# Kernel tuning notes

Hardware: AMD Instinct MI355X
Metric: run time of the kernel (lower is better)

The kernel has to match this reference:

```python
import jax, jax.numpy as jnp
import numpy as np

CAT = 19          # category_num + 1 (last slot is the catch-all cluster)
ATT_SCALE = float(np.sqrt(200.0))


def _layernorm(x, scale, bias, eps=1e-5):
    mu = jnp.mean(x, axis=-1, keepdims=True)
    var = jnp.mean((x - mu) ** 2, axis=-1, keepdims=True)
    return (x - mu) * jax.lax.rsqrt(var + eps) * scale + bias


def setup_inputs() -> dict:
    key = jax.random.key(0)
    ks = jax.random.split(key, 16)
    B, N, H, D, A, L = 64, 16, 100, 400, 200, 2
    nodes = H + (CAT - 1)  # 118
    s = 1.0 / np.sqrt(D)
    return {
        "history_embedding": jax.random.normal(ks[0], (B, H, D), jnp.float32),
        "candidate_news_representation": jax.random.normal(ks[1], (B, N, D), jnp.float32),
        "user_history_graph": jax.random.uniform(ks[2], (B, nodes, nodes), jnp.float32) / nodes,
        "user_history_category_mask": jax.random.randint(ks[3], (B, CAT), 0, 2, jnp.int32),
        "user_history_category_indices": jax.random.randint(ks[4], (B, H), 0, CAT, jnp.int32),
        "proxy_node_embedding": jax.random.normal(ks[5], (CAT - 1, D), jnp.float32) * 0.02,
        "gcn_W": jax.random.normal(ks[6], (L, D, D), jnp.float32) * s,
        "gcn_b": jnp.zeros((L, D), jnp.float32),
        "ln_scale": jnp.ones((L, D), jnp.float32),
        "ln_bias": jnp.zeros((L, D), jnp.float32),
        "Kw": jax.random.normal(ks[7], (D, A), jnp.float32) * s,
        "Qw": jax.random.normal(ks[8], (D, A), jnp.float32) * s,
        "Qb": jnp.zeros((A,), jnp.float32),
        "affine_W": jax.random.normal(ks[9], (D, D), jnp.float32) * s,
        "affine_b": jnp.zeros((D,), jnp.float32),
        "icKw": jax.random.normal(ks[10], (D, A), jnp.float32) * s,
        "icQw": jax.random.normal(ks[11], (D, A), jnp.float32) * s,
        "icQb": jnp.zeros((A,), jnp.float32),
    }


def _forward(history_embedding, candidate_news_representation, user_history_graph,
             proxy_node_embedding, gcn_W, gcn_b, ln_scale, ln_bias,
             Kw, Qw, Qb, affine_W, affine_b, icKw, icQw, icQb,
             user_history_category_mask, user_history_category_indices):
    B, H, D = history_embedding.shape
    N = candidate_news_representation.shape[1]
    L = gcn_W.shape[0]

    # append proxy cluster nodes to the history graph nodes (dropout = identity at eval)
    he = jnp.concatenate(
        [history_embedding, jnp.broadcast_to(proxy_node_embedding[None], (B, CAT - 1, D))],
        axis=1)  # [B, 118, D]

    # GCN with residual + layernorm per layer, then global residual
    h = he
    for l in range(L):
        z = jnp.einsum('bij,bjd->bid', user_history_graph, h) @ gcn_W[l] + gcn_b[l]
        z = jax.nn.relu(z) + h
        h = _layernorm(z, ln_scale[l], ln_bias[l])
    gcn_feat = (h + he)[:, :H]  # [B, H, D]

    # intra-cluster scatter softmax over history items grouped by category
    K = gcn_feat @ Kw                                     # [B, H, A]
    Q = candidate_news_representation @ Qw + Qb           # [B, N, A]
    a = jnp.einsum('bha,bna->bnh', K, Q) / ATT_SCALE      # [B, N, H]

    onehot = jax.nn.one_hot(user_history_category_indices, CAT, dtype=a.dtype)  # [B, H, C]
    seg = onehot.astype(bool)
    neg = jnp.finfo(a.dtype).min
    # segment-max for stable softmax: [B, N, H, C] -> max over H
    seg_max = jnp.where(seg[:, None], a[..., None], neg).max(axis=2)            # [B, N, C]
    a_shift = a - jnp.einsum('bhc,bnc->bnh', onehot, seg_max)
    e = jnp.exp(a_shift)
    denom = jnp.einsum('bhc,bnc->bnh', onehot, jnp.einsum('bnh,bhc->bnc', e, onehot))
    alpha = e / denom                                                           # [B, N, H]

    # scatter-sum of attention-weighted gcn features into category clusters
    weighted = alpha[..., None] * gcn_feat[:, None]                             # [B, N, H, D]
    intra = jnp.einsum('bnhd,bhc->bncd', weighted, onehot)                      # [B, N, C, D]
    intra = jax.nn.relu(intra @ affine_W + affine_b) + intra

    # inter-cluster scaled-dot-product candidate attention (last cluster always valid)
    mask = user_history_category_mask.at[:, -1].set(1).astype(bool)[:, None, :]  # [B, 1, C]
    Kf = intra @ icKw                                                           # [B, N, C, A]
    q = candidate_news_representation @ icQw + icQb                             # [B, N, A]
    s = jnp.einsum('bnca,bna->bnc', Kf, q) / ATT_SCALE
    w = jax.nn.softmax(jnp.where(mask, s, neg), axis=-1)
    return jnp.einsum('bnc,bncd->bnd', w, intra)                                # [B, N, D]


def reference(history_embedding, candidate_news_representation, user_history_graph,
              user_history_category_mask, user_history_category_indices,
              proxy_node_embedding, gcn_W, gcn_b, ln_scale, ln_bias,
              Kw, Qw, Qb, affine_W, affine_b, icKw, icQw, icQb):
    return _forward(history_embedding, candidate_news_representation, user_history_graph,
                    proxy_node_embedding, gcn_W, gcn_b, ln_scale, ln_bias,
                    Kw, Qw, Qb, affine_W, affine_b, icKw, icQw, icQb,
                    user_history_category_mask, user_history_category_indices)
```

## Files before the change

### kernel.cpp

```cpp
#include <hip/hip_runtime.h>
#include <hip/hip_bf16.h>
#include <math.h>

#define BB 64
#define NN 16
#define HH 100
#define DD 400
#define AA 200
#define CATN 19
#define NODES 118
#define BN (BB*NODES)
#define BH (BB*HH)
#define ATT_INV 0.07071067811865475f

typedef __attribute__((ext_vector_type(4))) float f32x4;
typedef __attribute__((ext_vector_type(8))) short s16x8;

__device__ __forceinline__ unsigned short f2bf(float f) {
  union { float f; unsigned int u; } v; v.f = f;
  unsigned int r = v.u + 0x7FFFu + ((v.u >> 16) & 1u);
  return (unsigned short)(r >> 16);
}
__device__ __forceinline__ float bf2f(unsigned short u) {
  union { unsigned int i; float f; } v; v.i = ((unsigned int)u) << 16; return v.f;
}

__global__ __launch_bounds__(256) void k_toT_he(const float* __restrict__ hist,
    const float* __restrict__ proxy, float* __restrict__ he,
    unsigned short* __restrict__ T) {
  __shared__ float t_sh[64][129];
  const int b = blockIdx.x / 7, dt = blockIdx.x % 7;
  const int d0 = dt * 64;
  const int tid = threadIdx.x;
  const int dc = tid & 63, jr = tid >> 6;
  for (int j0 = 0; j0 < 128; j0 += 4) {
    int j = j0 + jr, d = d0 + dc;
    float v = 0.f;
    if (j < NODES && d < DD) {
      v = (j < HH) ? hist[((size_t)b * HH + j) * DD + d]
                   : proxy[(size_t)(j - HH) * DD + d];
      he[((size_t)b * NODES + j) * DD + d] = v;
    }
    t_sh[dc][j] = v;
  }
  __syncthreads();
  const int jc = tid & 127, dr2 = tid >> 7;
  for (int di = 0; di < 64; di += 2) {
    int dr = di + dr2;
    int d = d0 + dr;
    if (d < 416) T[((size_t)b * 416 + d) * 128 + jc] = f2bf(t_sh[dr][jc]);
  }
}

template<int RPB>
__global__ __launch_bounds__(256) void k_toT(const float* __restrict__ h,
    unsigned short* __restrict__ T) {
  __shared__ float t_sh[64][129];
  const int b = blockIdx.x / 7, dt = blockIdx.x % 7;
  const int d0 = dt * 64;
  const int tid = threadIdx.x;
  const int dc = tid & 63, jr = tid >> 6;
  for (int j0 = 0; j0 < 128; j0 += 4) {
    int j = j0 + jr, d = d0 + dc;
    float v = (j < RPB && d < DD) ? h[((size_t)b * RPB + j) * DD + d] : 0.f;
    t_sh[dc][j] = v;
  }
  __syncthreads();
  const int jc = tid & 127, dr2 = tid >> 7;
  for (int di = 0; di < 64; di += 2) {
    int dr = di + dr2;
    int d = d0 + dr;
    if (d < 416) T[((size_t)b * 416 + d) * 128 + jc] = f2bf(t_sh[dr][jc]);
  }
}

__global__ __launch_bounds__(256) void k_toT_gf(const float* __restrict__ h2,
    const float* __restrict__ he, float* __restrict__ gf,
    unsigned short* __restrict__ T) {
  __shared__ float t_sh[64][129];
  const int b = blockIdx.x / 7, dt = blockIdx.x % 7;
  const int d0 = dt * 64;
  const int tid = threadIdx.x;
  const int dc = tid & 63, jr = tid >> 6;
  for (int j0 = 0; j0 < 128; j0 += 4) {
    int j = j0 + jr, d = d0 + dc;
    float v = 0.f;
    if (j < HH && d < DD) {
      size_t src = ((size_t)b * NODES + j) * DD + d;
      v = h2[src] + he[src];
      gf[((size_t)b * HH + j) * DD + d] = v;
    }
    t_sh[dc][j] = v;
  }
  __syncthreads();
  const int jc = tid & 127, dr2 = tid >> 7;
  for (int di = 0; di < 64; di += 2) {
    int dr = di + dr2;
    int d = d0 + dr;
    if (d < 416) T[((size_t)b * 416 + d) * 128 + jc] = f2bf(t_sh[dr][jc]);
  }
}

__global__ __launch_bounds__(256) void k_gmm(const float* __restrict__ G,
    const unsigned short* __restrict__ hT, unsigned short* __restrict__ tmpb) {
  __shared__ unsigned short a_sh[32 * 136];
  const int b = blockIdx.x >> 2;
  const int i0 = (blockIdx.x & 3) * 32;
  const int tid = threadIdx.x;
  for (int idx = tid; idx < 32 * 128; idx += 256) {
    int r = idx >> 7, j = idx & 127;
    int i = i0 + r;
    float v = (i < NODES && j < NODES) ? G[((size_t)b * NODES + i) * NODES + j] : 0.f;
    a_sh[r * 136 + j] = f2bf(v);
  }
  __syncthreads();
  const int lane = tid & 63, w = tid >> 6;
  const int lrow = lane & 15, lk = lane >> 4;
  const int rg = w & 1, nh = w >> 1;
  const int cbeg = nh * 13;
  f32x4 acc[13];
#pragma unroll
  for (int c = 0; c < 13; ++c) acc[c] = f32x4{0.f, 0.f, 0.f, 0.f};
  const unsigned short* ap = &a_sh[(rg * 16 + lrow) * 136 + lk * 8];
  const unsigned short* wp = &hT[((size_t)b * 416 + cbeg * 16 + lrow) * 128 + lk * 8];
  for (int ks = 0; ks < 4; ++ks) {
    s16x8 af = *reinterpret_cast<const s16x8*>(ap + ks * 32);
#pragma unroll
    for (int c = 0; c < 13; ++c) {
      s16x8 bf = *reinterpret_cast<const s16x8*>(wp + (size_t)c * 16 * 128 + ks * 32);
      acc[c] = __builtin_amdgcn_mfma_f32_16x16x32_bf16(af, bf, acc[c], 0, 0, 0);
    }
  }
  const int r0 = rg * 16 + lk * 4;
#pragma unroll
  for (int c = 0; c < 13; ++c) {
    int col = (cbeg + c) * 16 + lrow;
#pragma unroll
    for (int j = 0; j < 4; ++j) {
      int i = i0 + r0 + j;
      if (i < NODES)
        tmpb[((size_t)b * NODES + i) * 416 + col] = f2bf(acc[c][j]);
    }
  }
}

__global__ __launch_bounds__(256) void k_mgb_ln(
    const unsigned short* __restrict__ A, const unsigned short* __restrict__ Wt,
    const float* __restrict__ bias, const float* __restrict__ resid,
    const float* __restrict__ lns, const float* __restrict__ lnb,
    float* __restrict__ out) {
  __shared__ float ps_sh[32][2][2];
  const int tid = threadIdx.x;
  const size_t row0 = (size_t)blockIdx.x * 32;
  const int lane = tid & 63, w = tid >> 6;
  const int lrow = lane & 15, lk = lane >> 4;
  const int rg = w & 1, nh = w >> 1;
  const int cbeg = nh * 13;
  f32x4 acc[13];
#pragma unroll
  for (int c = 0; c < 13; ++c) acc[c] = f32x4{0.f, 0.f, 0.f, 0.f};
  const unsigned short* ap = &A[(row0 + rg * 16 + lrow) * 416 + lk * 8];
  const unsigned short* wp = &Wt[((size_t)(cbeg * 16) + lrow) * 416 + lk * 8];
  for (int ks = 0; ks < 13; ++ks) {
    s16x8 af = *reinterpret_cast<const s16x8*>(ap + ks * 32);
#pragma unroll
    for (int c = 0; c < 13; ++c) {
      s16x8 bf = *reinterpret_cast<const s16x8*>(wp + (size_t)c * 16 * 416 + ks * 32);
      acc[c] = __builtin_amdgcn_mfma_f32_16x16x32_bf16(af, bf, acc[c], 0, 0, 0);
    }
  }
  const int r0 = rg * 16 + lk * 4;
  float zs[4], zq[4];
#pragma unroll
  for (int j = 0; j < 4; ++j) { zs[j] = 0.f; zq[j] = 0.f; }
#pragma unroll
  for (int c = 0; c < 13; ++c) {
    int col = (cbeg + c) * 16 + lrow;
    bool cv = col < DD;
    float bv = cv ? bias[col] : 0.f;
#pragma unroll
    for (int j = 0; j < 4; ++j) {
      float z = 0.f;
      if (cv)
        z = fmaxf(acc[c][j] + bv, 0.f) + resid[(row0 + r0 + j) * (size_t)DD + col];
      acc[c][j] = z;
      zs[j] += z;
      zq[j] += z * z;
    }
  }
#pragma unroll
  for (int j = 0; j < 4; ++j) {
    zs[j] += __shfl_xor(zs[j], 1, 64); zq[j] += __shfl_xor(zq[j], 1, 64);
    zs[j] += __shfl_xor(zs[j], 2, 64); zq[j] += __shfl_xor(zq[j], 2, 64);
    zs[j] += __shfl_xor(zs[j], 4, 64); zq[j] += __shfl_xor(zq[j], 4, 64);
    zs[j] += __shfl_xor(zs[j], 8, 64); zq[j] += __shfl_xor(zq[j], 8, 64);
  }
  if (lrow == 0) {
#pragma unroll
    for (int j = 0; j < 4; ++j) {
      ps_sh[r0 + j][nh][0] = zs[j];
      ps_sh[r0 + j][nh][1] = zq[j];
    }
  }
  __syncthreads();
  float mu[4], rs[4];
#pragma unroll
  for (int j = 0; j < 4; ++j) {
    float s = ps_sh[r0 + j][0][0] + ps_sh[r0 + j][1][0];
    float q = ps_sh[r0 + j][0][1] + ps_sh[r0 + j][1][1];
    mu[j] = s * (1.0f / DD);
    float var = q * (1.0f / DD) - mu[j] * mu[j];
    rs[j] = 1.0f / sqrtf(var + 1e-5f);
  }
#pragma unroll
  for (int c = 0; c < 13; ++c) {
    int col = (cbeg + c) * 16 + lrow;
    if (col < DD) {
      float sc = lns[col], bo = lnb[col];
#pragma unroll
      for (int j = 0; j < 4; ++j)
        out[(row0 + r0 + j) * (size_t)DD + col] = (acc[c][j] - mu[j]) * rs[j] * sc + bo;
    }
  }
}

__global__ __launch_bounds__(256) void k_prep_all(const float* __restrict__ gW,
    const float* __restrict__ afW, const float* __restrict__ Kw,
    const float* __restrict__ Qw, const float* __restrict__ icQw,
    const float* __restrict__ icKw, const float* __restrict__ Qb,
    const float* __restrict__ icQb, unsigned short* __restrict__ wbase,
    float* __restrict__ bias3) {
  int idx = blockIdx.x * 256 + threadIdx.x;
  const int SG = 416 * 416;
  const int SK = 224 * 416;
  if (idx < SG) {
    int n = idx / 416, k = idx - n * 416;
    wbase[idx] = (n < 400 && k < 400) ? f2bf(gW[(size_t)k * 400 + n]) : (unsigned short)0;
    return;
  }
  idx -= SG;
  if (idx < SG) {
    int n = idx / 416, k = idx - n * 416;
    wbase[173056 + idx] = (n < 400 && k < 400) ? f2bf(gW[160000 + (size_t)k * 400 + n]) : (unsigned short)0;
    return;
  }
  idx -= SG;
  if (idx < SG) {
    int n = idx / 416, k = idx - n * 416;
    wbase[346112 + idx] = (n < 400 && k < 400) ? f2bf(afW[(size_t)k * 400 + n]) : (unsigned short)0;
    return;
  }
  idx -= SG;
  if (idx < SK) {
    int n = idx / 416, k = idx - n * 416;
    wbase[519168 + idx] = (n < 200 && k < 400) ? f2bf(Kw[(size_t)k * 200 + n]) : (unsigned short)0;
    return;
  }
  idx -= SK;
  if (idx < SK) {
    int d = idx / 224, a = idx - d * 224;
    wbase[612352 + idx] = (d < 400 && a < 200) ? f2bf(icKw[(size_t)d * 200 + a]) : (unsigned short)0;
    return;
  }
  idx -= SK;
  if (idx < SK) {
    int k = idx / 224, a = idx - k * 224;
    wbase[705536 + idx] = (k < 400 && a < 200) ? f2bf(icQw[(size_t)k * 200 + a]) : (unsigned short)0;
    return;
  }
  idx -= SK;
  if (idx < 208 * 416) {
    int n = idx / 416, k = idx - n * 416;
    wbase[798720 + idx] = (n < 200 && k < 400) ? f2bf(Qw[(size_t)k * 200 + n]) : (unsigned short)0;
    return;
  }
  idx -= 208 * 416;
  if (idx < 608) {
    float v = 0.f;
    if (idx < 200) v = Qb[idx];
    else if (idx >= 208) {
      const float* kr = icKw + (size_t)(idx - 208) * 200;
      float s = 0.f;
      for (int a = 0; a < 200; ++a) s += icQb[a] * kr[a];
      v = s;
    }
    bias3[idx] = v;
  }
}

__global__ __launch_bounds__(256) void k_prep_M(const unsigned short* __restrict__ icKwB,
    const unsigned short* __restrict__ icQwB, unsigned short* __restrict__ wqp) {
  const int tid = threadIdx.x;
  const size_t row0 = (size_t)blockIdx.x * 32;
  const int lane = tid & 63, w = tid >> 6;
  const int lrow = lane & 15, lk = lane >> 4;
  const int rg = w & 1, nh = w >> 1;
  const int cbeg = nh * 13;
  f32x4 acc[13];
#pragma unroll
  for (int c = 0; c < 13; ++c) acc[c] = f32x4{0.f, 0.f, 0.f, 0.f};
  const unsigned short* ap = &icKwB[(row0 + rg * 16 + lrow) * 224 + lk * 8];
  const unsigned short* bp = &icQwB[((size_t)(cbeg * 16) + lrow) * 224 + lk * 8];
  for (int ks = 0; ks < 7; ++ks) {
    s16x8 af = *reinterpret_cast<const s16x8*>(ap + ks * 32);
// ... 60 lines not shown
  }
  const int r0 = rg * 16 + lk * 4;
  if (EPI == 0) {
#pragma unroll
    for (int c = 0; c < NF0; ++c) {
      int col = (cbeg + c) * 16 + lrow;
      if (col < NOUT) {
#pragma unroll
        for (int j = 0; j < 4; ++j)
          out[(row0 + r0 + j) * (size_t)NOUT + col] = acc[c][j];
      }
    }
  } else {
#pragma unroll
    for (int c = 0; c < NF0; ++c) {
      int col = (cbeg + c) * 16 + lrow;
      if (col < 200) {
        float bv = bias[col];
#pragma unroll
        for (int j = 0; j < 4; ++j)
          out[(row0 + r0 + j) * (size_t)AA + col] = acc[c][j] + bv;
      } else if (col >= 208 && col < 608) {
        float bv = bias[col];
#pragma unroll
        for (int j = 0; j < 4; ++j)
          out2[(row0 + r0 + j) * (size_t)DD + (col - 208)] = acc[c][j] + bv;
      }
    }
  }
}

__global__ __launch_bounds__(256) void k_palpha(const float* __restrict__ K,
    const float* __restrict__ Q, const int* __restrict__ cat,
    unsigned short* __restrict__ P) {
  __shared__ float q_sh[AA];
  __shared__ float a_sh[HH];
  __shared__ int c_sh[HH];
  __shared__ float smax[CATN], sden[CATN];
  const int i = blockIdx.x;
  const int xcd = i & 7, s = i >> 3;
  const int b = 8 * xcd + (s >> 4);
  const int n = s & 15;
  const int bn = b * 16 + n;
  const int tid = threadIdx.x;
  if (tid < AA) q_sh[tid] = Q[(size_t)bn * AA + tid];
  if (tid < HH) c_sh[tid] = cat[b * HH + tid];
  __syncthreads();
  if (tid < 2 * HH) {
    int h = tid >> 1, half = tid & 1;
    const float* kp = K + ((size_t)b * HH + h) * AA + half * 100;
    const float* qp = q_sh + half * 100;
    float sv = 0.f;
#pragma unroll 4
    for (int a = 0; a < 100; ++a) sv += kp[a] * qp[a];
    sv += __shfl_xor(sv, 1, 64);
    if (half == 0) a_sh[h] = sv * ATT_INV;
  }
  __syncthreads();
  if (tid < CATN) {
    float m = -3.4e38f;
    for (int h = 0; h < HH; ++h)
      if (c_sh[h] == tid) m = fmaxf(m, a_sh[h]);
    smax[tid] = m;
  }
  __syncthreads();
  if (tid < HH) a_sh[tid] = expf(a_sh[tid] - smax[c_sh[tid]]);
  __syncthreads();
  if (tid < CATN) {
    float dsum = 0.f;
    for (int h = 0; h < HH; ++h)
      if (c_sh[h] == tid) dsum += a_sh[h];
    sden[tid] = dsum;
  }
  __syncthreads();
  if (tid < HH) a_sh[tid] = a_sh[tid] / sden[c_sh[tid]];
  __syncthreads();
  for (int idx = tid; idx < CATN * 128; idx += 256) {
    int c = idx >> 7, h = idx & 127;
    float v = (h < HH && c_sh[h] == c) ? a_sh[h] : 0.f;
    P[((size_t)b * 320 + n * CATN + c) * 128 + h] = f2bf(v);
  }
}

__global__ __launch_bounds__(128) void k_sc(const unsigned short* __restrict__ P,
    const unsigned short* __restrict__ gfT, unsigned short* __restrict__ intraB) {
  const int i = blockIdx.x;
  const int xcd = i & 7, s = i >> 3;
  const int b = 8 * xcd + s / CATN;
  const int t = s % CATN;
  const int tid = threadIdx.x;
  const int lane = tid & 63, w = tid >> 6;
  const int lrow = lane & 15, lk = lane >> 4;
  const int cbeg = w * 13;
  f32x4 acc[13];
#pragma unroll
  for (int c = 0; c < 13; ++c) acc[c] = f32x4{0.f, 0.f, 0.f, 0.f};
  const unsigned short* ap = &P[((size_t)b * 320 + t * 16 + lrow) * 128 + lk * 8];
  const unsigned short* wp = &gfT[((size_t)b * 416 + cbeg * 16 + lrow) * 128 + lk * 8];
  for (int ks = 0; ks < 4; ++ks) {
    s16x8 af = *reinterpret_cast<const s16x8*>(ap + ks * 32);
#pragma unroll
    for (int c = 0; c < 13; ++c) {
      s16x8 bf = *reinterpret_cast<const s16x8*>(wp + (size_t)c * 16 * 128 + ks * 32);
      acc[c] = __builtin_amdgcn_mfma_f32_16x16x32_bf16(af, bf, acc[c], 0, 0, 0);
    }
  }
  const int r0 = lk * 4;
#pragma unroll
  for (int c = 0; c < 13; ++c) {
    int col = (cbeg + c) * 16 + lrow;
#pragma unroll
    for (int j = 0; j < 4; ++j)
      intraB[((size_t)b * 304 + t * 16 + r0 + j) * 416 + col] =
          f2bf(col < DD ? acc[c][j] : 0.f);
  }
}

__global__ __launch_bounds__(256) void k_af(
    const unsigned short* __restrict__ A, const unsigned short* __restrict__ Wt,
    const float* __restrict__ bias, const float* __restrict__ p,
    float* __restrict__ s_pre, unsigned short* __restrict__ out2) {
  __shared__ float ps_sh[32][2];
  const int tid = threadIdx.x;
  const int g = (blockIdx.x % 8) * (gridDim.x / 8) + blockIdx.x / 8;
  const size_t row0 = (size_t)g * 32;
  const int lane = tid & 63, w = tid >> 6;
  const int lrow = lane & 15, lk = lane >> 4;
  const int rg = w & 1, nh = w >> 1;
  const int cbeg = nh * 13;
  f32x4 acc[13];
#pragma unroll
  for (int c = 0; c < 13; ++c) acc[c] = f32x4{0.f, 0.f, 0.f, 0.f};
  const unsigned short* ap = &A[(row0 + rg * 16 + lrow) * 416 + lk * 8];
  const unsigned short* wp = &Wt[((size_t)(cbeg * 16) + lrow) * 416 + lk * 8];
  for (int ks = 0; ks < 13; ++ks) {
    s16x8 af = *reinterpret_cast<const s16x8*>(ap + ks * 32);
#pragma unroll
    for (int c = 0; c < 13; ++c) {
      s16x8 bf = *reinterpret_cast<const s16x8*>(wp + (size_t)c * 16 * 416 + ks * 32);
      acc[c] = __builtin_amdgcn_mfma_f32_16x16x32_bf16(af, bf, acc[c], 0, 0, 0);
    }
  }
  const int r0 = rg * 16 + lk * 4;
  const float* prow[4];
#pragma unroll
  for (int j = 0; j < 4; ++j)
    prow[j] = p + (size_t)((row0 + r0 + j) / CATN) * DD;
  float spart[4] = {0.f, 0.f, 0.f, 0.f};
#pragma unroll
  for (int c = 0; c < 13; ++c) {
    int col = (cbeg + c) * 16 + lrow;
    if (col < DD) {
      float bv = bias[col];
#pragma unroll
      for (int j = 0; j < 4; ++j) {
        size_t row = row0 + r0 + j;
        float resid = bf2f(A[row * 416 + col]);
        float v = fmaxf(acc[c][j] + bv, 0.f) + resid;
        out2[row * 416 + col] = f2bf(v);
        spart[j] += v * prow[j][col];
      }
    }
  }
#pragma unroll
  for (int j = 0; j < 4; ++j) {
    spart[j] += __shfl_xor(spart[j], 1, 64);
    spart[j] += __shfl_xor(spart[j], 2, 64);
    spart[j] += __shfl_xor(spart[j], 4, 64);
    spart[j] += __shfl_xor(spart[j], 8, 64);
  }
  if (lrow == 0) {
#pragma unroll
    for (int j = 0; j < 4; ++j) ps_sh[r0 + j][nh] = spart[j];
  }
  __syncthreads();
  if (tid < 32)
    s_pre[row0 + tid] = (ps_sh[tid][0] + ps_sh[tid][1]) * ATT_INV;
}

__global__ __launch_bounds__(256) void k_final(const unsigned short* __restrict__ intra2B,
    const float* __restrict__ s_pre, const int* __restrict__ mask,
    float* __restrict__ out) {
  __shared__ float w_sh[CATN];
  const int i = blockIdx.x;
  const int xcd = i & 7, s = i >> 3;
  const int b = 8 * xcd + (s >> 4);
  const int n = s & 15;
  const int bn = b * 16 + n;
  const int tid = threadIdx.x;
  if (tid == 0) {
    float sv[CATN];
    float mx = -3.4e38f;
#pragma unroll
    for (int c = 0; c < CATN; ++c) {
      bool mk = (c == CATN - 1) || (mask[b * CATN + c] != 0);
      float sc = mk ? s_pre[bn * CATN + c] : -3.4e38f;
      sv[c] = sc;
      mx = fmaxf(mx, sc);
    }
    float den = 0.f;
#pragma unroll
    for (int c = 0; c < CATN; ++c) {
      float e = (sv[c] <= -3.3e38f) ? 0.f : expf(sv[c] - mx);
      w_sh[c] = e;
      den += e;
    }
    float inv = 1.0f / den;
#pragma unroll
    for (int c = 0; c < CATN; ++c) w_sh[c] *= inv;
  }
  __syncthreads();
  const unsigned short* ib = intra2B + (size_t)bn * CATN * 416;
  for (int d = tid; d < DD; d += 256) {
    float o = 0.f;
#pragma unroll
    for (int c = 0; c < CATN; ++c) o += w_sh[c] * bf2f(ib[c * 416 + d]);
    out[(size_t)bn * DD + d] = o;
  }
}

extern "C" void kernel_launch(void* const* d_in, const int* in_sizes, int n_in,
                              void* d_out, int out_size, void* d_ws, size_t ws_size,
                              hipStream_t stream) {
  const float* hist  = (const float*)d_in[0];
  const float* cand  = (const float*)d_in[1];
  const float* G     = (const float*)d_in[2];
  const int*   cmask = (const int*)d_in[3];
  const int*   cidx  = (const int*)d_in[4];
  const float* proxy = (const float*)d_in[5];
  const float* gW    = (const float*)d_in[6];
  const float* gb    = (const float*)d_in[7];
  const float* lns   = (const float*)d_in[8];
  const float* lnb   = (const float*)d_in[9];
  const float* Kw    = (const float*)d_in[10];
  const float* Qw    = (const float*)d_in[11];
  const float* Qbb   = (const float*)d_in[12];
  const float* afW   = (const float*)d_in[13];
  const float* afb   = (const float*)d_in[14];
  const float* icKw  = (const float*)d_in[15];
  const float* icQw  = (const float*)d_in[16];
  const float* icQb  = (const float*)d_in[17];
  float* out = (float*)d_out;
  float* ws  = (float*)d_ws;

  float* he    = ws;
  float* s1    = ws + 3020800;
  float* s2f   = ws + 6041600;
  unsigned short* tmpb   = (unsigned short*)(ws + 6041600);
  unsigned short* TB     = (unsigned short*)(ws + 9062400);
  unsigned short* intraB = (unsigned short*)(ws + 10766336);
  unsigned short* intra2B= (unsigned short*)(ws + 14813184);
  unsigned short* wbase  = (unsigned short*)(ws + 18860032);
  float* bias3 = ws + 19385856;
  unsigned short* Pbuf = (unsigned short*)ws;
  float* qbuf  = ws + 1310720;
  float* pbuf  = ws + 1515520;
  float* s_pre = ws + 1925120;
  float* Kbuf  = s1;
  unsigned short* gW0t  = wbase;
  unsigned short* gW1t  = wbase + 173056;
  unsigned short* afWt  = wbase + 346112;
  unsigned short* Kwt   = wbase + 519168;
  unsigned short* icKwB = wbase + 612352;
  unsigned short* icQwB = wbase + 705536;
  unsigned short* Wqp   = wbase + 798720;

  k_prep_all<<<3461, 256, 0, stream>>>(gW, afW, Kw, Qw, icQw, icKw, Qbb, icQb, wbase, bias3);
  k_prep_M<<<13, 256, 0, stream>>>(icKwB, icQwB, Wqp);
  k_toT_he<<<448, 256, 0, stream>>>(hist, proxy, he, TB);
  k_gmm<<<256, 256, 0, stream>>>(G, TB, tmpb);
  k_mgb_ln<<<BN / 32, 256, 0, stream>>>(tmpb, gW0t, gb, he, lns, lnb, s1);
  k_toT<NODES><<<448, 256, 0, stream>>>(s1, TB);
  k_gmm<<<256, 256, 0, stream>>>(G, TB, tmpb);
  k_mgb_ln<<<BN / 32, 256, 0, stream>>>(tmpb, gW1t, gb + DD, s1, lns + DD, lnb + DD, s1);
  k_toT_gf<<<448, 256, 0, stream>>>(s1, he, s2f, TB);
  k_mg<400, 416, 200, 0><<<BH / 32, 256, 0, stream>>>(s2f, Kwt, nullptr, Kbuf, nullptr);
  k_mg<400, 416, 608, 6><<<BB * NN / 32, 256, 0, stream>>>(cand, Wqp, bias3, qbuf, pbuf);
  k_palpha<<<BB * NN, 256, 0, stream>>>(Kbuf, qbuf, cidx, Pbuf);
  k_sc<<<BB * CATN, 128, 0, stream>>>(Pbuf, TB, intraB);
  k_af<<<BB * NN * CATN / 32, 256, 0, stream>>>(intraB, afWt, afb, pbuf, s_pre, intra2B);
  k_final<<<BB * NN, 256, 0, stream>>>(intra2B, s_pre, cmask, out);
}
```

Before: 337.9 us.

## Fuse graph matmul with GCN linear+LN and scatter matmul with affine

Merges the graph-propagation GEMM and the following weight GEMM with bias/ReLU/residual/LayerNorm into one kernel, keeping the intermediate tile in shared memory as bf16 instead of writing it to global memory. Likewise fuses the per-cluster scatter GEMM with the affine projection and score computation. This removes two intermediate global round trips and four kernel launches. In exchange the graph stage now uses 256 blocks instead of about 236 per GEMM, so there are fewer waves of parallelism, some padded rows waste work, and shared memory use per block grows.

```diff
diff --git a/kernel.cpp b/kernel.cpp
--- a/kernel.cpp
+++ b/kernel.cpp
@@ -101,75 +101,68 @@
   }
 }
 
-__global__ __launch_bounds__(256) void k_gmm(const float* __restrict__ G,
-    const unsigned short* __restrict__ hT, unsigned short* __restrict__ tmpb) {
-  __shared__ unsigned short a_sh[32 * 136];
-  const int b = blockIdx.x >> 2;
-  const int i0 = (blockIdx.x & 3) * 32;
-  const int tid = threadIdx.x;
+__global__ __launch_bounds__(256) void k_gln(const float* __restrict__ G,
+    const unsigned short* __restrict__ hT, const float* __restrict__ resid,
+    const unsigned short* __restrict__ Wt, const float* __restrict__ bias,
+    const float* __restrict__ lns, const float* __restrict__ lnb,
+    float* __restrict__ out) {
+  __shared__ unsigned short g_sh[32 * 136];
+  __shared__ unsigned short o_sh[32 * 424];
+  __shared__ float ps_sh[32][2][2];
+  const int tid = threadIdx.x;
+  const int g = (blockIdx.x & 7) * (gridDim.x >> 3) + (blockIdx.x >> 3);
+  const int b = g >> 2;
+  const int i0 = (g & 3) * 32;
   for (int idx = tid; idx < 32 * 128; idx += 256) {
     int r = idx >> 7, j = idx & 127;
     int i = i0 + r;
     float v = (i < NODES && j < NODES) ? G[((size_t)b * NODES + i) * NODES + j] : 0.f;
-    a_sh[r * 136 + j] = f2bf(v);
+    g_sh[r * 136 + j] = f2bf(v);
   }
   __syncthreads();
   const int lane = tid & 63, w = tid >> 6;
   const int lrow = lane & 15, lk = lane >> 4;
   const int rg = w & 1, nh = w >> 1;
   const int cbeg = nh * 13;
-  f32x4 acc[13];
-#pragma unroll
-  for (int c = 0; c < 13; ++c) acc[c] = f32x4{0.f, 0.f, 0.f, 0.f};
-  const unsigned short* ap = &a_sh[(rg * 16 + lrow) * 136 + lk * 8];
-  const unsigned short* wp = &hT[((size_t)b * 416 + cbeg * 16 + lrow) * 128 + lk * 8];
-  for (int ks = 0; ks < 4; ++ks) {
-    s16x8 af = *reinterpret_cast<const s16x8*>(ap + ks * 32);
+  const int r0 = rg * 16 + lk * 4;
+  {
+    f32x4 acc[13];
+#pragma unroll
+    for (int c = 0; c < 13; ++c) acc[c] = f32x4{0.f, 0.f, 0.f, 0.f};
+    const unsigned short* ap = &g_sh[(rg * 16 + lrow) * 136 + lk * 8];
+    const unsigned short* wp = &hT[((size_t)b * 416 + cbeg * 16 + lrow) * 128 + lk * 8];
+    for (int ks = 0; ks < 4; ++ks) {
+      s16x8 af = *reinterpret_cast<const s16x8*>(ap + ks * 32);
+#pragma unroll
+      for (int c = 0; c < 13; ++c) {
+        s16x8 bf = *reinterpret_cast<const s16x8*>(wp + (size_t)c * 16 * 128 + ks * 32);
+        acc[c] = __builtin_amdgcn_mfma_f32_16x16x32_bf16(af, bf, acc[c], 0, 0, 0);
+      }
+    }
 #pragma unroll
     for (int c = 0; c < 13; ++c) {
-      s16x8 bf = *reinterpret_cast<const s16x8*>(wp + (size_t)c * 16 * 128 + ks * 32);
-      acc[c] = __builtin_amdgcn_mfma_f32_16x16x32_bf16(af, bf, acc[c], 0, 0, 0);
-    }
-  }
-  const int r0 = rg * 16 + lk * 4;
-#pragma unroll
-  for (int c = 0; c < 13; ++c) {
-    int col = (cbeg + c) * 16 + lrow;
-#pragma unroll
-    for (int j = 0; j < 4; ++j) {
-      int i = i0 + r0 + j;
-      if (i < NODES)
-        tmpb[((size_t)b * NODES + i) * 416 + col] = f2bf(acc[c][j]);
-    }
-  }
-}
-
-__global__ __launch_bounds__(256) void k_mgb_ln(
-    const unsigned short* __restrict__ A, const unsigned short* __restrict__ Wt,
-    const float* __restrict__ bias, const float* __restrict__ resid,
-    const float* __restrict__ lns, const float* __restrict__ lnb,
-    float* __restrict__ out) {
-  __shared__ float ps_sh[32][2][2];
-  const int tid = threadIdx.x;
-  const size_t row0 = (size_t)blockIdx.x * 32;
-  const int lane = tid & 63, w = tid >> 6;
-  const int lrow = lane & 15, lk = lane >> 4;
-  const int rg = w & 1, nh = w >> 1;
-  const int cbeg = nh * 13;
-  f32x4 acc[13];
-#pragma unroll
-  for (int c = 0; c < 13; ++c) acc[c] = f32x4{0.f, 0.f, 0.f, 0.f};
-  const unsigned short* ap = &A[(row0 + rg * 16 + lrow) * 416 + lk * 8];
-  const unsigned short* wp = &Wt[((size_t)(cbeg * 16) + lrow) * 416 + lk * 8];
-  for (int ks = 0; ks < 13; ++ks) {
-    s16x8 af = *reinterpret_cast<const s16x8*>(ap + ks * 32);
-#pragma unroll
-    for (int c = 0; c < 13; ++c) {
-      s16x8 bf = *reinterpret_cast<const s16x8*>(wp + (size_t)c * 16 * 416 + ks * 32);
-      acc[c] = __builtin_amdgcn_mfma_f32_16x16x32_bf16(af, bf, acc[c], 0, 0, 0);
-    }
-  }
-  const int r0 = rg * 16 + lk * 4;
+      int col = (cbeg + c) * 16 + lrow;
+#pragma unroll
+      for (int j = 0; j < 4; ++j)
+        o_sh[(r0 + j) * 424 + col] = f2bf(acc[c][j]);
+    }
+  }
+  __syncthreads();
+  f32x4 acc2[13];
+#pragma unroll
+  for (int c = 0; c < 13; ++c) acc2[c] = f32x4{0.f, 0.f, 0.f, 0.f};
+  {
+    const unsigned short* ap = &o_sh[(rg * 16 + lrow) * 424 + lk * 8];
+    const unsigned short* wp = &Wt[((size_t)(cbeg * 16) + lrow) * 416 + lk * 8];
+    for (int ks = 0; ks < 13; ++ks) {
+      s16x8 af = *reinterpret_cast<const s16x8*>(ap + ks * 32);
+#pragma unroll
+      for (int c = 0; c < 13; ++c) {
+        s16x8 bf = *reinterpret_cast<const s16x8*>(wp + (size_t)c * 16 * 416 + ks * 32);
+        acc2[c] = __builtin_amdgcn_mfma_f32_16x16x32_bf16(af, bf, acc2[c], 0, 0, 0);
+      }
+    }
+  }
   float zs[4], zq[4];
 #pragma unroll
   for (int j = 0; j < 4; ++j) { zs[j] = 0.f; zq[j] = 0.f; }
@@ -180,10 +173,11 @@
     float bv = cv ? bias[col] : 0.f;
 #pragma unroll
     for (int j = 0; j < 4; ++j) {
+      int i = i0 + r0 + j;
       float z = 0.f;
-      if (cv)
-        z = fmaxf(acc[c][j] + bv, 0.f) + resid[(row0 + r0 + j) * (size_t)DD + col];
-      acc[c][j] = z;
+      if (cv && i < NODES)
+        z = fmaxf(acc2[c][j] + bv, 0.f) + resid[((size_t)b * NODES + i) * DD + col];
+      acc2[c][j] = z;
       zs[j] += z;
       zq[j] += z * z;
     }
@@ -207,9 +201,9 @@
 #pragma unroll
   for (int j = 0; j < 4; ++j) {
     float s = ps_sh[r0 + j][0][0] + ps_sh[r0 + j][1][0];
-    float q = ps_sh[r0 + j][0][1] + ps_sh[r0 + j][1][1];
+    float q2 = ps_sh[r0 + j][0][1] + ps_sh[r0 + j][1][1];
     mu[j] = s * (1.0f / DD);
-    float var = q * (1.0f / DD) - mu[j] * mu[j];
+    float var = q2 * (1.0f / DD) - mu[j] * mu[j];
     rs[j] = 1.0f / sqrtf(var + 1e-5f);
   }
 #pragma unroll
@@ -218,8 +212,11 @@
     if (col < DD) {
       float sc = lns[col], bo = lnb[col];
 #pragma unroll
-      for (int j = 0; j < 4; ++j)
-        out[(row0 + r0 + j) * (size_t)DD + col] = (acc[c][j] - mu[j]) * rs[j] * sc + bo;
+      for (int j = 0; j < 4; ++j) {
+        int i = i0 + r0 + j;
+        if (i < NODES)
+          out[((size_t)b * NODES + i) * DD + col] = (acc2[c][j] - mu[j]) * rs[j] * sc + bo;
+      }
     }
   }
 }
@@ -446,100 +443,101 @@
   }
 }
 
-__global__ __launch_bounds__(128) void k_sc(const unsigned short* __restrict__ P,
-    const unsigned short* __restrict__ gfT, unsigned short* __restrict__ intraB) {
-  const int i = blockIdx.x;
-  const int xcd = i & 7, s = i >> 3;
-  const int b = 8 * xcd + s / CATN;
-  const int t = s % CATN;
-  const int tid = threadIdx.x;
-  const int lane = tid & 63, w = tid >> 6;
-  const int lrow = lane & 15, lk = lane >> 4;
-  const int cbeg = w * 13;
-  f32x4 acc[13];
-#pragma unroll
-  for (int c = 0; c < 13; ++c) acc[c] = f32x4{0.f, 0.f, 0.f, 0.f};
-  const unsigned short* ap = &P[((size_t)b * 320 + t * 16 + lrow) * 128 + lk * 8];
-  const unsigned short* wp = &gfT[((size_t)b * 416 + cbeg * 16 + lrow) * 128 + lk * 8];
-  for (int ks = 0; ks < 4; ++ks) {
-    s16x8 af = *reinterpret_cast<const s16x8*>(ap + ks * 32);
-#pragma unroll
-    for (int c = 0; c < 13; ++c) {
-      s16x8 bf = *reinterpret_cast<const s16x8*>(wp + (size_t)c * 16 * 128 + ks * 32);
-      acc[c] = __builtin_amdgcn_mfma_f32_16x16x32_bf16(af, bf, acc[c], 0, 0, 0);
-    }
-  }
-  const int r0 = lk * 4;
-#pragma unroll
-  for (int c = 0; c < 13; ++c) {
-    int col = (cbeg + c) * 16 + lrow;
-#pragma unroll
-    for (int j = 0; j < 4; ++j)
-      intraB[((size_t)b * 304 + t * 16 + r0 + j) * 416 + col] =
-          f2bf(col < DD ? acc[c][j] : 0.f);
-  }
-}
-
-__global__ __launch_bounds__(256) void k_af(
-    const unsigned short* __restrict__ A, const unsigned short* __restrict__ Wt,
-    const float* __restrict__ bias, const float* __restrict__ p,
-    float* __restrict__ s_pre, unsigned short* __restrict__ out2) {
+__global__ __launch_bounds__(256) void k_scaf(
+    const unsigned short* __restrict__ P, const unsigned short* __restrict__ gfT,
+    const unsigned short* __restrict__ afWt, const float* __restrict__ afb,
+    const float* __restrict__ p, float* __restrict__ s_pre,
+    unsigned short* __restrict__ intra2B) {
+  __shared__ unsigned short o_sh[32 * 424];
   __shared__ float ps_sh[32][2];
   const int tid = threadIdx.x;
-  const int g = (blockIdx.x % 8) * (gridDim.x / 8) + blockIdx.x / 8;
-  const size_t row0 = (size_t)g * 32;
+  const int g = (blockIdx.x & 7) * (gridDim.x >> 3) + (blockIdx.x >> 3);
+  const int b = g / 10;
+  const int r0p = (g - b * 10) * 32;
   const int lane = tid & 63, w = tid >> 6;
   const int lrow = lane & 15, lk = lane >> 4;
   const int rg = w & 1, nh = w >> 1;
   const int cbeg = nh * 13;
-  f32x4 acc[13];
-#pragma unroll
-  for (int c = 0; c < 13; ++c) acc[c] = f32x4{0.f, 0.f, 0.f, 0.f};
-  const unsigned short* ap = &A[(row0 + rg * 16 + lrow) * 416 + lk * 8];
-  const unsigned short* wp = &Wt[((size_t)(cbeg * 16) + lrow) * 416 + lk * 8];
-  for (int ks = 0; ks < 13; ++ks) {
-    s16x8 af = *reinterpret_cast<const s16x8*>(ap + ks * 32);
+  const int r0 = rg * 16 + lk * 4;
+  {
+    f32x4 acc[13];
+#pragma unroll
+    for (int c = 0; c < 13; ++c) acc[c] = f32x4{0.f, 0.f, 0.f, 0.f};
+    const unsigned short* ap = &P[((size_t)b * 320 + r0p + rg * 16 + lrow) * 128 + lk * 8];
+    const unsigned short* wp = &gfT[((size_t)b * 416 + cbeg * 16 + lrow) * 128 + lk * 8];
+    for (int ks = 0; ks < 4; ++ks) {
+      s16x8 af = *reinterpret_cast<const s16x8*>(ap + ks * 32);
+#pragma unroll
+      for (int c = 0; c < 13; ++c) {
+        s16x8 bf = *reinterpret_cast<const s16x8*>(wp + (size_t)c * 16 * 128 + ks * 32);
+        acc[c] = __builtin_amdgcn_mfma_f32_16x16x32_bf16(af, bf, acc[c], 0, 0, 0);
+      }
+    }
 #pragma unroll
     for (int c = 0; c < 13; ++c) {
-      s16x8 bf = *reinterpret_cast<const s16x8*>(wp + (size_t)c * 16 * 416 + ks * 32);
-      acc[c] = __builtin_amdgcn_mfma_f32_16x16x32_bf16(af, bf, acc[c], 0, 0, 0);
-    }
-  }
-  const int r0 = rg * 16 + lk * 4;
+      int col = (cbeg + c) * 16 + lrow;
+#pragma unroll
+      for (int j = 0; j < 4; ++j) {
+        int pr = r0p + r0 + j;
+        o_sh[(r0 + j) * 424 + col] = f2bf((pr < 304 && col < DD) ? acc[c][j] : 0.f);
+      }
+    }
+  }
+  __syncthreads();
+  f32x4 acc2[13];
+#pragma unroll
+  for (int c = 0; c < 13; ++c) acc2[c] = f32x4{0.f, 0.f, 0.f, 0.f};
+  {
+    const unsigned short* ap = &o_sh[(rg * 16 + lrow) * 424 + lk * 8];
+    const unsigned short* wp = &afWt[((size_t)(cbeg * 16) + lrow) * 416 + lk * 8];
+    for (int ks = 0; ks < 13; ++ks) {
+      s16x8 af = *reinterpret_cast<const s16x8*>(ap + ks * 32);
+#pragma unroll
+      for (int c = 0; c < 13; ++c) {
+        s16x8 bf = *reinterpret_cast<const s16x8*>(wp + (size_t)c * 16 * 416 + ks * 32);
+        acc2[c] = __builtin_amdgcn_mfma_f32_16x16x32_bf16(af, bf, acc2[c], 0, 0, 0);
+      }
+    }
+  }
   const float* prow[4];
 #pragma unroll
-  for (int j = 0; j < 4; ++j)
-    prow[j] = p + (size_t)((row0 + r0 + j) / CATN) * DD;
-  float spart[4] = {0.f, 0.f, 0.f, 0.f};
+  for (int j = 0; j < 4; ++j) {
+    int prc = r0p + r0 + j;
+    if (prc > 303) prc = 303;
+    prow[j] = p + (size_t)(b * 16 + prc / CATN) * DD;
+  }
+  float sp[4] = {0.f, 0.f, 0.f, 0.f};
 #pragma unroll
   for (int c = 0; c < 13; ++c) {
     int col = (cbeg + c) * 16 + lrow;
     if (col < DD) {
-      float bv = bias[col];
+      float bv = afb[col];
 #pragma unroll
       for (int j = 0; j < 4; ++j) {
-        size_t row = row0 + r0 + j;
-        float resid = bf2f(A[row * 416 + col]);
-        float v = fmaxf(acc[c][j] + bv, 0.f) + resid;
-        out2[row * 416 + col] = f2bf(v);
-        spart[j] += v * prow[j][col];
+        int pr = r0p + r0 + j;
+        if (pr < 304) {
+          size_t grow = (size_t)b * 304 + pr;
+          float v = fmaxf(acc2[c][j] + bv, 0.f) + bf2f(o_sh[(r0 + j) * 424 + col]);
+          intra2B[grow * 416 + col] = f2bf(v);
+          sp[j] += v * prow[j][col];
+        }
       }
     }
   }
 #pragma unroll
   for (int j = 0; j < 4; ++j) {
-    spart[j] += __shfl_xor(spart[j], 1, 64);
-    spart[j] += __shfl_xor(spart[j], 2, 64);
-    spart[j] += __shfl_xor(spart[j], 4, 64);
-    spart[j] += __shfl_xor(spart[j], 8, 64);
+    sp[j] += __shfl_xor(sp[j], 1, 64);
+    sp[j] += __shfl_xor(sp[j], 2, 64);
+    sp[j] += __shfl_xor(sp[j], 4, 64);
+    sp[j] += __shfl_xor(sp[j], 8, 64);
   }
   if (lrow == 0) {
 #pragma unroll
-    for (int j = 0; j < 4; ++j) ps_sh[r0 + j][nh] = spart[j];
-  }
-  __syncthreads();
-  if (tid < 32)
-    s_pre[row0 + tid] = (ps_sh[tid][0] + ps_sh[tid][1]) * ATT_INV;
+    for (int j = 0; j < 4; ++j) ps_sh[r0 + j][nh] = sp[j];
+  }
+  __syncthreads();
+  if (tid < 32 && r0p + tid < 304)
+    s_pre[(size_t)b * 304 + r0p + tid] = (ps_sh[tid][0] + ps_sh[tid][1]) * ATT_INV;
 }
 
 __global__ __launch_bounds__(256) void k_final(const unsigned short* __restrict__ intra2B,
@@ -610,9 +608,7 @@
   float* he    = ws;
   float* s1    = ws + 3020800;
   float* s2f   = ws + 6041600;
-  unsigned short* tmpb   = (unsigned short*)(ws + 6041600);
   unsigned short* TB     = (unsigned short*)(ws + 9062400);
-  unsigned short* intraB = (unsigned short*)(ws + 10766336);
   unsigned short* intra2B= (unsigned short*)(ws + 14813184);
   unsigned short* wbase  = (unsigned short*)(ws + 18860032);
   float* bias3 = ws + 19385856;
@@ -632,16 +628,13 @@
   k_prep_all<<<3461, 256, 0, stream>>>(gW, afW, Kw, Qw, icQw, icKw, Qbb, icQb, wbase, bias3);
   k_prep_M<<<13, 256, 0, stream>>>(icKwB, icQwB, Wqp);
   k_toT_he<<<448, 256, 0, stream>>>(hist, proxy, he, TB);
-  k_gmm<<<256, 256, 0, stream>>>(G, TB, tmpb);
-  k_mgb_ln<<<BN / 32, 256, 0, stream>>>(tmpb, gW0t, gb, he, lns, lnb, s1);
+  k_gln<<<256, 256, 0, stream>>>(G, TB, he, gW0t, gb, lns, lnb, s1);
   k_toT<NODES><<<448, 256, 0, stream>>>(s1, TB);
-  k_gmm<<<256, 256, 0, stream>>>(G, TB, tmpb);
-  k_mgb_ln<<<BN / 32, 256, 0, stream>>>(tmpb, gW1t, gb + DD, s1, lns + DD, lnb + DD, s1);
+  k_gln<<<256, 256, 0, stream>>>(G, TB, s1, gW1t, gb + DD, lns + DD, lnb + DD, s1);
   k_toT_gf<<<448, 256, 0, stream>>>(s1, he, s2f, TB);
   k_mg<400, 416, 200, 0><<<BH / 32, 256, 0, stream>>>(s2f, Kwt, nullptr, Kbuf, nullptr);
   k_mg<400, 416, 608, 6><<<BB * NN / 32, 256, 0, stream>>>(cand, Wqp, bias3, qbuf, pbuf);
   k_palpha<<<BB * NN, 256, 0, stream>>>(Kbuf, qbuf, cidx, Pbuf);
-  k_sc<<<BB * CATN, 128, 0, stream>>>(Pbuf, TB, intraB);
-  k_af<<<BB * NN * CATN / 32, 256, 0, stream>>>(intraB, afWt, afb, pbuf, s_pre, intra2B);
+  k_scaf<<<640, 256, 0, stream>>>(Pbuf, TB, afWt, afb, pbuf, s_pre, intra2B);
   k_final<<<BB * NN, 256, 0, stream>>>(intra2B, s_pre, cmask, out);
 }
```

Result: slower. 453.4 us (+34.2%).

## Halve row tile to 16 in GCN and affine MFMA kernels, doubling block count

Applied to the files above, without the earlier changes.

Reworks k_gmm, k_mgb_ln, k_sc and the affine kernel so each 256-thread block handles 16 rows, with four waves each taking 7 column tiles instead of 13. Grid sizes double, which spreads the work across more CUs, and k_gmm now uses an XCD-aware block remap. The cost is that weight-tile loads are repeated across twice as many blocks, and the LayerNorm and score reductions now sum over four waves.

```diff
diff --git a/kernel.cpp b/kernel.cpp
--- a/kernel.cpp
+++ b/kernel.cpp
@@ -103,11 +103,12 @@
 
 __global__ __launch_bounds__(256) void k_gmm(const float* __restrict__ G,
     const unsigned short* __restrict__ hT, unsigned short* __restrict__ tmpb) {
-  __shared__ unsigned short a_sh[32 * 136];
-  const int b = blockIdx.x >> 2;
-  const int i0 = (blockIdx.x & 3) * 32;
-  const int tid = threadIdx.x;
-  for (int idx = tid; idx < 32 * 128; idx += 256) {
+  __shared__ unsigned short a_sh[16 * 136];
+  const int tid = threadIdx.x;
+  const int g = (blockIdx.x & 7) * (gridDim.x >> 3) + (blockIdx.x >> 3);
+  const int b = g >> 3;
+  const int i0 = (g & 7) * 16;
+  for (int idx = tid; idx < 16 * 128; idx += 256) {
     int r = idx >> 7, j = idx & 127;
     int i = i0 + r;
     float v = (i < NODES && j < NODES) ? G[((size_t)b * NODES + i) * NODES + j] : 0.f;
@@ -116,30 +117,30 @@
   __syncthreads();
   const int lane = tid & 63, w = tid >> 6;
   const int lrow = lane & 15, lk = lane >> 4;
-  const int rg = w & 1, nh = w >> 1;
-  const int cbeg = nh * 13;
-  f32x4 acc[13];
-#pragma unroll
-  for (int c = 0; c < 13; ++c) acc[c] = f32x4{0.f, 0.f, 0.f, 0.f};
-  const unsigned short* ap = &a_sh[(rg * 16 + lrow) * 136 + lk * 8];
+  const int cbeg = w * 7;
+  f32x4 acc[7];
+#pragma unroll
+  for (int c = 0; c < 7; ++c) acc[c] = f32x4{0.f, 0.f, 0.f, 0.f};
+  const unsigned short* ap = &a_sh[lrow * 136 + lk * 8];
   const unsigned short* wp = &hT[((size_t)b * 416 + cbeg * 16 + lrow) * 128 + lk * 8];
   for (int ks = 0; ks < 4; ++ks) {
     s16x8 af = *reinterpret_cast<const s16x8*>(ap + ks * 32);
 #pragma unroll
-    for (int c = 0; c < 13; ++c) {
+    for (int c = 0; c < 7; ++c) {
       s16x8 bf = *reinterpret_cast<const s16x8*>(wp + (size_t)c * 16 * 128 + ks * 32);
       acc[c] = __builtin_amdgcn_mfma_f32_16x16x32_bf16(af, bf, acc[c], 0, 0, 0);
     }
   }
-  const int r0 = rg * 16 + lk * 4;
-#pragma unroll
-  for (int c = 0; c < 13; ++c) {
+#pragma unroll
+  for (int c = 0; c < 7; ++c) {
     int col = (cbeg + c) * 16 + lrow;
-#pragma unroll
-    for (int j = 0; j < 4; ++j) {
-      int i = i0 + r0 + j;
-      if (i < NODES)
-        tmpb[((size_t)b * NODES + i) * 416 + col] = f2bf(acc[c][j]);
+    if (col < 416) {
+#pragma unroll
+      for (int j = 0; j < 4; ++j) {
+        int i = i0 + lk * 4 + j;
+        if (i < NODES)
+          tmpb[((size_t)b * NODES + i) * 416 + col] = f2bf(acc[c][j]);
+      }
     }
   }
 }
@@ -149,32 +150,31 @@
     const float* __restrict__ bias, const float* __restrict__ resid,
     const float* __restrict__ lns, const float* __restrict__ lnb,
     float* __restrict__ out) {
-  __shared__ float ps_sh[32][2][2];
-  const int tid = threadIdx.x;
-  const size_t row0 = (size_t)blockIdx.x * 32;
+  __shared__ float ps_sh[16][4][2];
+  const int tid = threadIdx.x;
+  const int g = (blockIdx.x % 8) * (gridDim.x / 8) + blockIdx.x / 8;
+  const size_t row0 = (size_t)g * 16;
   const int lane = tid & 63, w = tid >> 6;
   const int lrow = lane & 15, lk = lane >> 4;
-  const int rg = w & 1, nh = w >> 1;
-  const int cbeg = nh * 13;
-  f32x4 acc[13];
-#pragma unroll
-  for (int c = 0; c < 13; ++c) acc[c] = f32x4{0.f, 0.f, 0.f, 0.f};
-  const unsigned short* ap = &A[(row0 + rg * 16 + lrow) * 416 + lk * 8];
+  const int cbeg = w * 7;
+  f32x4 acc[7];
+#pragma unroll
+  for (int c = 0; c < 7; ++c) acc[c] = f32x4{0.f, 0.f, 0.f, 0.f};
+  const unsigned short* ap = &A[(row0 + lrow) * 416 + lk * 8];
   const unsigned short* wp = &Wt[((size_t)(cbeg * 16) + lrow) * 416 + lk * 8];
   for (int ks = 0; ks < 13; ++ks) {
     s16x8 af = *reinterpret_cast<const s16x8*>(ap + ks * 32);
 #pragma unroll
-    for (int c = 0; c < 13; ++c) {
+    for (int c = 0; c < 7; ++c) {
       s16x8 bf = *reinterpret_cast<const s16x8*>(wp + (size_t)c * 16 * 416 + ks * 32);
       acc[c] = __builtin_amdgcn_mfma_f32_16x16x32_bf16(af, bf, acc[c], 0, 0, 0);
     }
   }
-  const int r0 = rg * 16 + lk * 4;
   float zs[4], zq[4];
 #pragma unroll
   for (int j = 0; j < 4; ++j) { zs[j] = 0.f; zq[j] = 0.f; }
 #pragma unroll
-  for (int c = 0; c < 13; ++c) {
+  for (int c = 0; c < 7; ++c) {
     int col = (cbeg + c) * 16 + lrow;
     bool cv = col < DD;
     float bv = cv ? bias[col] : 0.f;
@@ -182,7 +182,7 @@
     for (int j = 0; j < 4; ++j) {
       float z = 0.f;
       if (cv)
-        z = fmaxf(acc[c][j] + bv, 0.f) + resid[(row0 + r0 + j) * (size_t)DD + col];
+        z = fmaxf(acc[c][j] + bv, 0.f) + resid[(row0 + lk * 4 + j) * (size_t)DD + col];
       acc[c][j] = z;
       zs[j] += z;
       zq[j] += z * z;
@@ -198,28 +198,28 @@
   if (lrow == 0) {
 #pragma unroll
     for (int j = 0; j < 4; ++j) {
-      ps_sh[r0 + j][nh][0] = zs[j];
-      ps_sh[r0 + j][nh][1] = zq[j];
+      ps_sh[lk * 4 + j][w][0] = zs[j];
+      ps_sh[lk * 4 + j][w][1] = zq[j];
     }
   }
   __syncthreads();
   float mu[4], rs[4];
 #pragma unroll
   for (int j = 0; j < 4; ++j) {
-    float s = ps_sh[r0 + j][0][0] + ps_sh[r0 + j][1][0];
-    float q = ps_sh[r0 + j][0][1] + ps_sh[r0 + j][1][1];
+    int la = lk * 4 + j;
+    float s = ps_sh[la][0][0] + ps_sh[la][1][0] + ps_sh[la][2][0] + ps_sh[la][3][0];
+    float q = ps_sh[la][0][1] + ps_sh[la][1][1] + ps_sh[la][2][1] + ps_sh[la][3][1];
     mu[j] = s * (1.0f / DD);
-    float var = q * (1.0f / DD) - mu[j] * mu[j];
-    rs[j] = 1.0f / sqrtf(var + 1e-5f);
-  }
-#pragma unroll
-  for (int c = 0; c < 13; ++c) {
+    rs[j] = 1.0f / sqrtf(q * (1.0f / DD) - mu[j] * mu[j] + 1e-5f);
+  }
+#pragma unroll
+  for (int c = 0; c < 7; ++c) {
     int col = (cbeg + c) * 16 + lrow;
     if (col < DD) {
       float sc = lns[col], bo = lnb[col];
 #pragma unroll
       for (int j = 0; j < 4; ++j)
-        out[(row0 + r0 + j) * (size_t)DD + col] = (acc[c][j] - mu[j]) * rs[j] * sc + bo;
+        out[(row0 + lk * 4 + j) * (size_t)DD + col] = (acc[c][j] - mu[j]) * rs[j] * sc + bo;
     }
   }
 }
@@ -446,7 +446,7 @@
   }
 }
 
-__global__ __launch_bounds__(128) void k_sc(const unsigned short* __restrict__ P,
+__global__ __launch_bounds__(256) void k_sc(const unsigned short* __restrict__ P,
     const unsigned short* __restrict__ gfT, unsigned short* __restrict__ intraB) {
   const int i = blockIdx.x;
   const int xcd = i & 7, s = i >> 3;
@@ -455,91 +455,90 @@
   const int tid = threadIdx.x;
   const int lane = tid & 63, w = tid >> 6;
   const int lrow = lane & 15, lk = lane >> 4;
-  const int cbeg = w * 13;
-  f32x4 acc[13];
-#pragma unroll
-  for (int c = 0; c < 13; ++c) acc[c] = f32x4{0.f, 0.f, 0.f, 0.f};
+  const int cbeg = w * 7;
+  f32x4 acc[7];
+#pragma unroll
+  for (int c = 0; c < 7; ++c) acc[c] = f32x4{0.f, 0.f, 0.f, 0.f};
   const unsigned short* ap = &P[((size_t)b * 320 + t * 16 + lrow) * 128 + lk * 8];
   const unsigned short* wp = &gfT[((size_t)b * 416 + cbeg * 16 + lrow) * 128 + lk * 8];
   for (int ks = 0; ks < 4; ++ks) {
     s16x8 af = *reinterpret_cast<const s16x8*>(ap + ks * 32);
 #pragma unroll
-    for (int c = 0; c < 13; ++c) {
+    for (int c = 0; c < 7; ++c) {
       s16x8 bf = *reinterpret_cast<const s16x8*>(wp + (size_t)c * 16 * 128 + ks * 32);
       acc[c] = __builtin_amdgcn_mfma_f32_16x16x32_bf16(af, bf, acc[c], 0, 0, 0);
     }
   }
-  const int r0 = lk * 4;
-#pragma unroll
-  for (int c = 0; c < 13; ++c) {
+#pragma unroll
+  for (int c = 0; c < 7; ++c) {
     int col = (cbeg + c) * 16 + lrow;
-#pragma unroll
-    for (int j = 0; j < 4; ++j)
-      intraB[((size_t)b * 304 + t * 16 + r0 + j) * 416 + col] =
-          f2bf(col < DD ? acc[c][j] : 0.f);
-  }
-}
-
-__global__ __launch_bounds__(256) void k_af(
+    if (col < 416) {
+#pragma unroll
+      for (int j = 0; j < 4; ++j)
+        intraB[((size_t)b * 304 + t * 16 + lk * 4 + j) * 416 + col] =
+            f2bf(col < DD ? acc[c][j] : 0.f);
+    }
+  }
+}
+
+__global__ __launch_bounds__(256) void k_afq(
     const unsigned short* __restrict__ A, const unsigned short* __restrict__ Wt,
     const float* __restrict__ bias, const float* __restrict__ p,
     float* __restrict__ s_pre, unsigned short* __restrict__ out2) {
-  __shared__ float ps_sh[32][2];
+  __shared__ float ps_sh[16][4];
   const int tid = threadIdx.x;
   const int g = (blockIdx.x % 8) * (gridDim.x / 8) + blockIdx.x / 8;
-  const size_t row0 = (size_t)g * 32;
+  const size_t row0 = (size_t)g * 16;
   const int lane = tid & 63, w = tid >> 6;
   const int lrow = lane & 15, lk = lane >> 4;
-  const int rg = w & 1, nh = w >> 1;
-  const int cbeg = nh * 13;
-  f32x4 acc[13];
-#pragma unroll
-  for (int c = 0; c < 13; ++c) acc[c] = f32x4{0.f, 0.f, 0.f, 0.f};
-  const unsigned short* ap = &A[(row0 + rg * 16 + lrow) * 416 + lk * 8];
+  const int cbeg = w * 7;
+  f32x4 acc[7];
+#pragma unroll
+  for (int c = 0; c < 7; ++c) acc[c] = f32x4{0.f, 0.f, 0.f, 0.f};
+  const unsigned short* ap = &A[(row0 + lrow) * 416 + lk * 8];
   const unsigned short* wp = &Wt[((size_t)(cbeg * 16) + lrow) * 416 + lk * 8];
   for (int ks = 0; ks < 13; ++ks) {
     s16x8 af = *reinterpret_cast<const s16x8*>(ap + ks * 32);
 #pragma unroll
-    for (int c = 0; c < 13; ++c) {
+    for (int c = 0; c < 7; ++c) {
       s16x8 bf = *reinterpret_cast<const s16x8*>(wp + (size_t)c * 16 * 416 + ks * 32);
       acc[c] = __builtin_amdgcn_mfma_f32_16x16x32_bf16(af, bf, acc[c], 0, 0, 0);
     }
   }
-  const int r0 = rg * 16 + lk * 4;
   const float* prow[4];
 #pragma unroll
   for (int j = 0; j < 4; ++j)
-    prow[j] = p + (size_t)((row0 + r0 + j) / CATN) * DD;
-  float spart[4] = {0.f, 0.f, 0.f, 0.f};
-#pragma unroll
-  for (int c = 0; c < 13; ++c) {
+    prow[j] = p + (size_t)((row0 + lk * 4 + j) / CATN) * DD;
+  float sp[4] = {0.f, 0.f, 0.f, 0.f};
+#pragma unroll
+  for (int c = 0; c < 7; ++c) {
     int col = (cbeg + c) * 16 + lrow;
     if (col < DD) {
       float bv = bias[col];
 #pragma unroll
       for (int j = 0; j < 4; ++j) {
-        size_t row = row0 + r0 + j;
-        float resid = bf2f(A[row * 416 + col]);
-        float v = fmaxf(acc[c][j] + bv, 0.f) + resid;
-        out2[row * 416 + col] = f2bf(v);
-        spart[j] += v * prow[j][col];
+        size_t ra = row0 + lk * 4 + j;
+        float v = fmaxf(acc[c][j] + bv, 0.f) + bf2f(A[ra * 416 + col]);
+        out2[ra * 416 + col] = f2bf(v);
+        sp[j] += v * prow[j][col];
       }
     }
   }
 #pragma unroll
   for (int j = 0; j < 4; ++j) {
-    spart[j] += __shfl_xor(spart[j], 1, 64);
-    spart[j] += __shfl_xor(spart[j], 2, 64);
-    spart[j] += __shfl_xor(spart[j], 4, 64);
-    spart[j] += __shfl_xor(spart[j], 8, 64);
+    sp[j] += __shfl_xor(sp[j], 1, 64);
+    sp[j] += __shfl_xor(sp[j], 2, 64);
+    sp[j] += __shfl_xor(sp[j], 4, 64);
+    sp[j] += __shfl_xor(sp[j], 8, 64);
   }
   if (lrow == 0) {
 #pragma unroll
-    for (int j = 0; j < 4; ++j) ps_sh[r0 + j][nh] = spart[j];
-  }
-  __syncthreads();
-  if (tid < 32)
-    s_pre[row0 + tid] = (ps_sh[tid][0] + ps_sh[tid][1]) * ATT_INV;
+    for (int j = 0; j < 4; ++j) ps_sh[lk * 4 + j][w] = sp[j];
+  }
+  __syncthreads();
+  if (tid < 16)
+    s_pre[row0 + tid] =
+        (ps_sh[tid][0] + ps_sh[tid][1] + ps_sh[tid][2] + ps_sh[tid][3]) * ATT_INV;
 }
 
 __global__ __launch_bounds__(256) void k_final(const unsigned short* __restrict__ intra2B,
@@ -632,16 +631,16 @@
   k_prep_all<<<3461, 256, 0, stream>>>(gW, afW, Kw, Qw, icQw, icKw, Qbb, icQb, wbase, bias3);
   k_prep_M<<<13, 256, 0, stream>>>(icKwB, icQwB, Wqp);
   k_toT_he<<<448, 256, 0, stream>>>(hist, proxy, he, TB);
-  k_gmm<<<256, 256, 0, stream>>>(G, TB, tmpb);
-  k_mgb_ln<<<BN / 32, 256, 0, stream>>>(tmpb, gW0t, gb, he, lns, lnb, s1);
+  k_gmm<<<512, 256, 0, stream>>>(G, TB, tmpb);
+  k_mgb_ln<<<BN / 16, 256, 0, stream>>>(tmpb, gW0t, gb, he, lns, lnb, s1);
   k_toT<NODES><<<448, 256, 0, stream>>>(s1, TB);
-  k_gmm<<<256, 256, 0, stream>>>(G, TB, tmpb);
-  k_mgb_ln<<<BN / 32, 256, 0, stream>>>(tmpb, gW1t, gb + DD, s1, lns + DD, lnb + DD, s1);
+  k_gmm<<<512, 256, 0, stream>>>(G, TB, tmpb);
+  k_mgb_ln<<<BN / 16, 256, 0, stream>>>(tmpb, gW1t, gb + DD, s1, lns + DD, lnb + DD, s1);
   k_toT_gf<<<448, 256, 0, stream>>>(s1, he, s2f, TB);
   k_mg<400, 416, 200, 0><<<BH / 32, 256, 0, stream>>>(s2f, Kwt, nullptr, Kbuf, nullptr);
   k_mg<400, 416, 608, 6><<<BB * NN / 32, 256, 0, stream>>>(cand, Wqp, bias3, qbuf, pbuf);
   k_palpha<<<BB * NN, 256, 0, stream>>>(Kbuf, qbuf, cidx, Pbuf);
-  k_sc<<<BB * CATN, 128, 0, stream>>>(Pbuf, TB, intraB);
-  k_af<<<BB * NN * CATN / 32, 256, 0, stream>>>(intraB, afWt, afb, pbuf, s_pre, intra2B);
+  k_sc<<<BB * CATN, 256, 0, stream>>>(Pbuf, TB, intraB);
+  k_afq<<<BB * NN * CATN / 16, 256, 0, stream>>>(intraB, afWt, afb, pbuf, s_pre, intra2B);
   k_final<<<BB * NN, 256, 0, stream>>>(intra2B, s_pre, cmask, out);
 }
```

Result: faster. 311.5 us (-7.8%).
